# Kernel tuning notes

Measured on AMD Instinct MI355X. Metric: run time of the kernel, lower is better.

The kernel has to match this reference:

```python
import jax, jax.numpy as jnp
import numpy as np

N_NODES = 50000
N_EDGES = 800000
HIDDEN = 128
NUM_RBF = 32
N_GRAPHS = 500
VOCAB = 100


def setup_inputs() -> dict:
    key = jax.random.key(0)
    ks = jax.random.split(key, 16)
    x = jax.random.randint(ks[0], (N_NODES,), 0, VOCAB)
    edge_index = jax.random.randint(ks[1], (2, N_EDGES), 0, N_NODES)
    edge_attr = jax.random.normal(ks[2], (N_EDGES, NUM_RBF), dtype=jnp.float32)
    batch = jnp.sort(jax.random.randint(ks[3], (N_NODES,), 0, N_GRAPHS))
    zdim = 2 * HIDDEN + NUM_RBF
    s = 1.0 / np.sqrt(zdim)
    params = {"emb": jax.random.normal(ks[4], (VOCAB, HIDDEN), dtype=jnp.float32)}
    for l, k0 in zip((1, 2, 3), (5, 8, 11)):
        params[f"Wf{l}"] = jax.random.uniform(ks[k0], (zdim, HIDDEN), minval=-s, maxval=s, dtype=jnp.float32)
        params[f"bf{l}"] = jnp.zeros((HIDDEN,), dtype=jnp.float32)
        params[f"Ws{l}"] = jax.random.uniform(ks[k0 + 1], (zdim, HIDDEN), minval=-s, maxval=s, dtype=jnp.float32)
        params[f"bs{l}"] = jnp.zeros((HIDDEN,), dtype=jnp.float32)
    sl = 1.0 / np.sqrt(HIDDEN)
    params["Wlin"] = jax.random.uniform(ks[14], (HIDDEN, HIDDEN), minval=-sl, maxval=sl, dtype=jnp.float32)
    params["blin"] = jnp.zeros((HIDDEN,), dtype=jnp.float32)
    return {"x": x, "edge_index": edge_index, "edge_attr": edge_attr, "batch": batch, **params}


def _cgconv(h, src, dst, edge_attr, Wf, bf, Ws, bs):
    # z = [x_i || x_j || e_ij]; i = target (dst), j = source (src)
    z = jnp.concatenate([h[dst], h[src], edge_attr], axis=-1)  # [E, 2H+D]
    msg = jax.nn.sigmoid(z @ Wf + bf) * jax.nn.softplus(z @ Ws + bs)  # [E, H]
    agg = jax.ops.segment_sum(msg, dst, num_segments=N_NODES)
    return h + agg


def reference(x, edge_index, edge_attr, batch, emb,
              Wf1, bf1, Ws1, bs1, Wf2, bf2, Ws2, bs2, Wf3, bf3, Ws3, bs3,
              Wlin, blin):
    src, dst = edge_index[0], edge_index[1]
    h = emb[x]  # [N, H]
    h = jax.nn.relu(_cgconv(h, src, dst, edge_attr, Wf1, bf1, Ws1, bs1))
    h = jax.nn.relu(_cgconv(h, src, dst, edge_attr, Wf2, bf2, Ws2, bs2))
    h = jax.nn.relu(_cgconv(h, src, dst, edge_attr, Wf3, bf3, Ws3, bs3))
    sums = jax.ops.segment_sum(h, batch, num_segments=N_GRAPHS)  # [G, H]
    counts = jax.ops.segment_sum(jnp.ones((N_NODES,), h.dtype), batch, num_segments=N_GRAPHS)
    pooled = sums / jnp.maximum(counts, 1.0)[:, None]
    return pooled @ Wlin + blin
```

## Files before the change

### kernel.cpp

```cpp
#include <hip/hip_runtime.h>
#include <hip/hip_bf16.h>
#include <hip/hip_fp16.h>
#include <cstdint>
#include <cstddef>

#define NNODES 50000
#define NEDGES 800000
#define HID 128
#define NRBF 32
#define NGRAPH 500
#define NB_SCAN 196
#define EPB 64
#define NEBLK (NEDGES / EPB)
#define SROW 130

typedef __attribute__((ext_vector_type(8))) short short8;
typedef __attribute__((ext_vector_type(4))) float f32x4;

__device__ inline short f2bf(float x) {
  __hip_bfloat16 b = __float2bfloat16(x);
  return *reinterpret_cast<short*>(&b);
}

__device__ inline unsigned int pk_bf16(float a, float b) {
  unsigned int r;
  asm("v_cvt_pk_bf16_f32 %0, %1, %2" : "=v"(r) : "v"(a), "v"(b));
  return r;
}
__device__ inline unsigned int pk_f16(float a, float b) {
  unsigned int r;
  asm("v_cvt_pkrtz_f16_f32 %0, %1, %2" : "=v"(r) : "v"(a), "v"(b));
  return r;
}
__device__ inline unsigned int pk_add_f16(unsigned int a, unsigned int b) {
  unsigned int r;
  asm("v_pk_add_f16 %0, %1, %2" : "=v"(r) : "v"(a), "v"(b));
  return r;
}
__device__ inline float aexp2(float x) {
  float r;
  asm("v_exp_f32 %0, %1" : "=v"(r) : "v"(x));
  return r;
}
__device__ inline float alog2(float x) {
  float r;
  asm("v_log_f32 %0, %1" : "=v"(r) : "v"(x));
  return r;
}

#define SC_F (-1.4426950408889634f)
#define SC_S (1.4426950408889634f)

__global__ void prep_all(
    const float* __restrict__ Wf0, const float* __restrict__ Ws0,
    const float* __restrict__ bf0, const float* __restrict__ bs0,
    const float* __restrict__ Wf1, const float* __restrict__ Ws1,
    const float* __restrict__ bf1, const float* __restrict__ bs1,
    const float* __restrict__ Wf2, const float* __restrict__ Ws2,
    const float* __restrict__ bf2, const float* __restrict__ bs2,
    unsigned short* __restrict__ WtB3, unsigned short* __restrict__ WnB3,
    float* __restrict__ biasv3) {
  const int l = blockIdx.y;
  const float* Wf = (l == 0) ? Wf0 : ((l == 1) ? Wf1 : Wf2);
  const float* Ws = (l == 0) ? Ws0 : ((l == 1) ? Ws1 : Ws2);
  const float* bf = (l == 0) ? bf0 : ((l == 1) ? bf1 : bf2);
  const float* bs = (l == 0) ? bs0 : ((l == 1) ? bs1 : bs2);
  unsigned short* WtB = WtB3 + l * 8192;
  unsigned short* WnB = WnB3 + l * 65536;
  float* biasv = biasv3 + l * 256;

  int i0 = blockIdx.x * blockDim.x + threadIdx.x;
  if (i0 < 8192) {
    int i = i0;
    int j = i & 7, lane = (i >> 3) & 63, t = i >> 9;
    int q = lane >> 4, n = lane & 15;
    int k = q * 8 + j, c = (t & 7) * 16 + n;
    const float* W = (t < 8) ? Wf : Ws;
    const float sc = (t < 8) ? SC_F : SC_S;
    WtB[i] = (unsigned short)f2bf(W[(size_t)(256 + k) * HID + c] * sc);
  } else if (i0 < 8192 + 65536) {
    int i = i0 - 8192;
    int j = i & 7;
    int lane = (i >> 3) & 63;
    int tk = (i >> 9) & 3;
    int tc = i >> 11;
    int q = lane >> 4, n = lane & 15;
    int k = tk * 32 + q * 8 + j;
    float v;
    int which;
    if (tc < 16) {
      int g = tc >> 1;
      which = tc & 1;
      int c = g * 16 + n;
      const float* W = which ? Ws : Wf;
      v = W[(size_t)k * HID + c];
    } else {
      int g = (tc - 16) >> 1;
      which = (tc - 16) & 1;
      int c = g * 16 + n;
      const float* W = which ? Ws : Wf;
      v = W[(size_t)(128 + k) * HID + c];
    }
    WnB[i] = (unsigned short)f2bf(v * (which ? SC_S : SC_F));
    if (i < 256) {
      int c2 = i >> 1, w2 = i & 1;
      biasv[i] = w2 ? bs[c2] * SC_S : bf[c2] * SC_F;
    }
  }
}

__global__ void deg_hist(const int* __restrict__ dst, int* __restrict__ deg) {
  int e = blockIdx.x * blockDim.x + threadIdx.x;
  if (e < NEDGES) atomicAdd(&deg[dst[e]], 1);
}

__global__ __launch_bounds__(256) void scan_block(const int* __restrict__ deg, int* __restrict__ bsum) {
  __shared__ int s[256];
  int i = blockIdx.x * 256 + threadIdx.x;
  s[threadIdx.x] = (i < NNODES) ? deg[i] : 0;
  __syncthreads();
  for (int off = 128; off > 0; off >>= 1) {
    if (threadIdx.x < off) s[threadIdx.x] += s[threadIdx.x + off];
    __syncthreads();
  }
  if (threadIdx.x == 0) bsum[blockIdx.x] = s[0];
}

__global__ __launch_bounds__(256) void scan_top(const int* __restrict__ bsum,
                                                int* __restrict__ bpre) {
  __shared__ int s[256];
  int t = threadIdx.x;
  int v = (t < NB_SCAN) ? bsum[t] : 0;
  s[t] = v;
  __syncthreads();
  for (int off = 1; off < 256; off <<= 1) {
    int u = (t >= off) ? s[t - off] : 0;
    __syncthreads();
    s[t] += u;
    __syncthreads();
  }
  if (t < NB_SCAN) bpre[t] = s[t] - v;
}

__global__ __launch_bounds__(256) void scan_final(const int* __restrict__ deg,
                                                  const int* __restrict__ bpre,
                                                  int* __restrict__ cursor) {
  __shared__ int s[256];
  int i = blockIdx.x * 256 + threadIdx.x;
  int v = (i < NNODES) ? deg[i] : 0;
  s[threadIdx.x] = v;
  __syncthreads();
  for (int off = 1; off < 256; off <<= 1) {
    int t = (threadIdx.x >= off) ? s[threadIdx.x - off] : 0;
    __syncthreads();
    s[threadIdx.x] += t;
    __syncthreads();
  }
  if (i < NNODES) cursor[i] = bpre[blockIdx.x] + s[threadIdx.x] - v;
}

__global__ void scatter_edges_pack(const int* __restrict__ src, const int* __restrict__ dst,
                                   const float* __restrict__ eattr, int* __restrict__ cursor,
                                   int2* __restrict__ se2, unsigned short* __restrict__ eaB) {
  int e = blockIdx.x * blockDim.x + threadIdx.x;
  if (e >= NEDGES) return;
  int d = dst[e];
  int pos = atomicAdd(&cursor[d], 1);
  se2[pos] = make_int2(src[e], d);
  const float* ep = eattr + (size_t)e * NRBF;
  unsigned short* op = eaB + (size_t)pos * NRBF;
#pragma unroll
  for (int part = 0; part < 4; ++part) {
    const float4 v0 = *(const float4*)&ep[part * 8];
    const float4 v1 = *(const float4*)&ep[part * 8 + 4];
    uint4 o;
    o.x = pk_bf16(v0.x, v0.y);
    o.y = pk_bf16(v0.z, v0.w);
    o.z = pk_bf16(v1.x, v1.y);
    o.w = pk_bf16(v1.z, v1.w);
    *(uint4*)&op[part * 8] = o;
  }
}

__global__ __launch_bounds__(256) void node_mfma(
    const int* __restrict__ x, const float* __restrict__ emb,
    float* __restrict__ h, float* __restrict__ agg,
    const unsigned short* __restrict__ WnB, const float* __restrict__ biasv,
    unsigned int* __restrict__ Pdst, unsigned int* __restrict__ Psrc, int mode, int N) {
  const int tid = threadIdx.x;
  const int wv = tid >> 6;
  const int lane = tid & 63;
  const int q = lane >> 4;
  const int n = lane & 15;
  const int nb = blockIdx.x * 32 + (wv >> 1) * 16;
  const int srcwave = wv & 1;
  const int ctile0 = srcwave * 16;

  const bool valid = (nb + n) < N;
  int anode = nb + n;
  if (anode >= N) anode = N - 1;
  float* hp = h + (size_t)anode * HID;

  short8 a[4];
  if (mode == 0) {
    const float* ep = emb + (size_t)x[anode] * HID;
#pragma unroll
    for (int kt = 0; kt < 4; ++kt) {
      const float4 e0 = *(const float4*)&ep[kt * 32 + q * 8];
      const float4 e1 = *(const float4*)&ep[kt * 32 + q * 8 + 4];
      if (valid && !srcwave) {
        *(float4*)&hp[kt * 32 + q * 8] = e0;
        *(float4*)&hp[kt * 32 + q * 8 + 4] = e1;
      }
      union { short8 s8; unsigned int u32[4]; } au;
      au.u32[0] = pk_bf16(e0.x, e0.y);
      au.u32[1] = pk_bf16(e0.z, e0.w);
      au.u32[2] = pk_bf16(e1.x, e1.y);
      au.u32[3] = pk_bf16(e1.z, e1.w);
      a[kt] = au.s8;
    }
  } else {
    float* ap = agg + (size_t)anode * HID;
    float4 ev[8];
#pragma unroll
    for (int kt = 0; kt < 4; ++kt) {
      float4 e0 = *(const float4*)&hp[kt * 32 + q * 8];
      float4 e1 = *(const float4*)&hp[kt * 32 + q * 8 + 4];
      const float4 g0 = *(const float4*)&ap[kt * 32 + q * 8];
      const float4 g1 = *(const float4*)&ap[kt * 32 + q * 8 + 4];
      e0.x = fmaxf(e0.x + g0.x, 0.f); e0.y = fmaxf(e0.y + g0.y, 0.f);
      e0.z = fmaxf(e0.z + g0.z, 0.f); e0.w = fmaxf(e0.w + g0.w, 0.f);
      e1.x = fmaxf(e1.x + g1.x, 0.f); e1.y = fmaxf(e1.y + g1.y, 0.f);
      e1.z = fmaxf(e1.z + g1.z, 0.f); e1.w = fmaxf(e1.w + g1.w, 0.f);
      ev[2 * kt] = e0;
      ev[2 * kt + 1] = e1;
      union { short8 s8; unsigned int u32[4]; } au;
      au.u32[0] = pk_bf16(e0.x, e0.y);
      au.u32[1] = pk_bf16(e0.z, e0.w);
      au.u32[2] = pk_bf16(e1.x, e1.y);
      au.u32[3] = pk_bf16(e1.z, e1.w);
      a[kt] = au.s8;
    }
    __syncthreads();
    if (valid && !srcwave) {
      const float4 z4 = {0.f, 0.f, 0.f, 0.f};
#pragma unroll
      for (int kt = 0; kt < 4; ++kt) {
        *(float4*)&hp[kt * 32 + q * 8] = ev[2 * kt];
        *(float4*)&hp[kt * 32 + q * 8 + 4] = ev[2 * kt + 1];
        *(float4*)&ap[kt * 32 + q * 8] = z4;
        *(float4*)&ap[kt * 32 + q * 8 + 4] = z4;
      }
    }
  }

  const short8* WnB8 = (const short8*)WnB;
  f32x4 acc[16];
#pragma unroll
  for (int tc = 0; tc < 16; ++tc) acc[tc] = (f32x4){0.f, 0.f, 0.f, 0.f};

#pragma unroll
  for (int tc = 0; tc < 16; ++tc) {
#pragma unroll
    for (int kt = 0; kt < 4; ++kt) {
      short8 b = WnB8[((size_t)((ctile0 + tc) * 4 + kt)) * 64 + lane];
      acc[tc] = __builtin_amdgcn_mfma_f32_16x16x32_bf16(a[kt], b, acc[tc], 0, 0, 0);
    }
  }

  if (!srcwave) {
#pragma unroll
    for (int g2 = 0; g2 < 8; ++g2) {
      const int c = g2 * 16 + n;
      const float bvf = biasv[2 * c];
      const float bvs = biasv[2 * c + 1];
#pragma unroll
      for (int r = 0; r < 4; ++r) {
        int nd = nb + q * 4 + r;
        if (nd < N)
          Pdst[(size_t)nd * 128 + c] = pk_f16(acc[2 * g2][r] + bvf, acc[2 * g2 + 1][r] + bvs);
      }
    }
  } else {
#pragma unroll
    for (int g2 = 0; g2 < 8; ++g2) {
      const int c = g2 * 16 + n;
#pragma unroll
      for (int r = 0; r < 4; ++r) {
        int nd = nb + q * 4 + r;
        if (nd < N) Psrc[(size_t)nd * 128 + c] = pk_f16(acc[2 * g2][r], acc[2 * g2 + 1][r]);
      }
    }
  }
}

__global__ __launch_bounds__(256) void edge_mfma(
    const unsigned int* __restrict__ Pdst, const unsigned int* __restrict__ Psrc,
    const unsigned short* __restrict__ eaB, const unsigned short* __restrict__ WtB,
    const int2* __restrict__ se2, float* __restrict__ agg) {
  __shared__ unsigned int fsL[EPB * SROW];
  __shared__ int dstL[EPB];
  __shared__ int grpStart[EPB + 1];
  __shared__ int sndS;

  const int tid = threadIdx.x;
  const int base = blockIdx.x * EPB;
  const int lane = tid & 63;

  if (tid < EPB) {
    int2 sd = se2[base + tid];
    dstL[tid] = sd.y;
    int d = sd.y;
    int dprev = __shfl_up(d, 1);
    int flag = (tid == 0 || dprev != d) ? 1 : 0;
    unsigned long long mask = __ballot(flag);
    unsigned long long below = (lane == 63) ? ~0ull : ((1ull << (lane + 1)) - 1);
    int slot = __popcll(mask & below) - 1;
    if (flag) grpStart[slot] = tid;
    if (tid == 0) {
      int nd = __popcll(mask);
      sndS = nd;
      grpStart[nd] = EPB;
    }
  }

  const int wv = tid >> 6;
  const int q = lane >> 4;
  const int n = lane & 15;
  const int rowb = wv * 16 + q * 4;

  const short8 afrag = *(const short8*)&eaB[(size_t)(base + wv * 16 + n) * 32 + q * 8];

  const unsigned int* pp[4];
  const unsigned int* dp[4];
#pragma unroll
  for (int r = 0; r < 4; ++r) {
    const int2 sd = se2[base + rowb + r];
    pp[r] = Psrc + (size_t)sd.x * 128 + n;
    dp[r] = Pdst + (size_t)sd.y * 128 + n;
  }

  const short8* WtB8 = (const short8*)WtB;
  const f32x4 zero4 = {0.f, 0.f, 0.f, 0.f};
#pragma unroll
  for (int t = 0; t < 8; ++t) {
    unsigned int zpk[4];
#pragma unroll
    for (int r = 0; r < 4; ++r) zpk[r] = pk_add_f16(pp[r][t * 16], dp[r][t * 16]);
    short8 bfr = WtB8[t * 64 + lane];
    short8 bsr = WtB8[(8 + t) * 64 + lane];
    f32x4 cf = __builtin_amdgcn_mfma_f32_16x16x32_bf16(afrag, bfr, zero4, 0, 0, 0);
    f32x4 cs = __builtin_amdgcn_mfma_f32_16x16x32_bf16(afrag, bsr, zero4, 0, 0, 0);
#pragma unroll
    for (int r = 0; r < 4; ++r) {
      fsL[(rowb + r) * SROW + t * 16 + n] = pk_add_f16(pk_f16(cf[r], cs[r]), zpk[r]);
    }
  }
  __syncthreads();

  const int nd = sndS;
  for (int g = wv; g < nd; g += 4) {
    const int jb = grpStart[g];
    const int je = grpStart[g + 1];
    const int d = __builtin_amdgcn_readfirstlane(dstL[jb]);
    float acc0 = 0.f, acc1 = 0.f;

    uint2 pk_nx = *(const uint2*)&fsL[jb * SROW + 2 * lane];
    for (int j = jb; j < je; ++j) {
      const uint2 pk = pk_nx;
      int jn = (j + 1 < je) ? (j + 1) : j;
      pk_nx = *(const uint2*)&fsL[jn * SROW + 2 * lane];

      const float2 z0 = __half22float2(*reinterpret_cast<const __half2*>(&pk.x));
      const float2 z1 = __half22float2(*reinterpret_cast<const __half2*>(&pk.y));
      const float sig0 = __builtin_amdgcn_rcpf(1.f + aexp2(z0.x));
      const float sig1 = __builtin_amdgcn_rcpf(1.f + aexp2(z1.x));
      const float sp0 = fmaxf(z0.y, 0.f) + alog2(1.f + aexp2(fminf(z0.y, -z0.y)));
      const float sp1 = fmaxf(z1.y, 0.f) + alog2(1.f + aexp2(fminf(z1.y, -z1.y)));
      acc0 = fmaf(sig0, sp0, acc0);
      acc1 = fmaf(sig1, sp1, acc1);
    }
    acc0 *= 0.6931471805599453f;
    acc1 *= 0.6931471805599453f;
    float* ap = agg + (size_t)d * HID + 2 * lane;
    if (g == 0 || g == nd - 1) {
      atomicAdd(ap, acc0);
      atomicAdd(ap + 1, acc1);
    } else {
      *(float2*)ap = make_float2(acc0, acc1);
    }
  }
}

__global__ __launch_bounds__(256) void pool_kernel(
    const float* __restrict__ h, const float* __restrict__ agg,
    const int* __restrict__ batch, float* __restrict__ sums, float* __restrict__ counts) {
  __shared__ int gidL[64];
  __shared__ int grpS[65];
  __shared__ int sndP;

  const int tid = threadIdx.x;
  const int lane = tid & 63;
  const int wv = tid >> 6;
  const int nb = blockIdx.x * 64;
  int nvalid = NNODES - nb;
  if (nvalid > 64) nvalid = 64;

  if (tid < 64) {
    int node = nb + tid;
    int g = batch[node < NNODES ? node : NNODES - 1];
    gidL[tid] = g;
    int gprev = __shfl_up(g, 1);
    int flag = (tid < nvalid && (tid == 0 || gprev != g)) ? 1 : 0;
    unsigned long long mask = __ballot(flag);
    int slot = __popcll(mask & ((lane == 63) ? ~0ull : ((1ull << (lane + 1)) - 1))) - 1;
    if (flag) grpS[slot] = tid;
    if (tid == 0) {
      int nd = __popcll(mask);
      sndP = nd;
      grpS[nd] = nvalid;
    }
  }
  __syncthreads();

  const int nd = sndP;
  for (int g = wv; g < nd; g += 4) {
    const int jb = grpS[g];
    const int je = grpS[g + 1];
    const int gid = __builtin_amdgcn_readfirstlane(gidL[jb]);
    float a0 = 0.f, a1 = 0.f;
    for (int j = jb; j < je; ++j) {
      const float2 hv = *(const float2*)&h[(size_t)(nb + j) * HID + 2 * lane];
      const float2 av = *(const float2*)&agg[(size_t)(nb + j) * HID + 2 * lane];
      a0 += fmaxf(hv.x + av.x, 0.f);
      a1 += fmaxf(hv.y + av.y, 0.f);
    }
    float* sp = sums + (size_t)gid * HID + 2 * lane;
    const bool bnd = (g == 0 || g == nd - 1);
    if (bnd) {
      atomicAdd(sp, a0);
      atomicAdd(sp + 1, a1);
    } else {
      *(float2*)sp = make_float2(a0, a1);
    }
    if (lane == 0) {
      if (bnd) atomicAdd(&counts[gid], (float)(je - jb));
      else counts[gid] = (float)(je - jb);
    }
  }
}

__global__ __launch_bounds__(128) void final_kernel(
    const float* __restrict__ sums, const float* __restrict__ counts,
    const float* __restrict__ Wlin, const float* __restrict__ blin,
    float* __restrict__ out) {
  int g = blockIdx.x;
  int c = threadIdx.x;
  __shared__ float pool[HID];
  float cnt = counts[g];
  cnt = cnt > 1.f ? cnt : 1.f;
  pool[c] = sums[(size_t)g * HID + c] / cnt;
  __syncthreads();
  float acc = blin[c];
#pragma unroll 8
  for (int k = 0; k < HID; ++k) acc = fmaf(pool[k], Wlin[k * HID + c], acc);
  out[(size_t)g * HID + c] = acc;
}

extern "C" void kernel_launch(void* const* d_in, const int* in_sizes, int n_in,
                              void* d_out, int out_size, void* d_ws, size_t ws_size,
                              hipStream_t stream) {
  const int* x = (const int*)d_in[0];
  const int* eidx = (const int*)d_in[1];
  const float* eattr = (const float*)d_in[2];
  const int* batch = (const int*)d_in[3];
  const float* emb = (const float*)d_in[4];
  const float* Wf[3] = {(const float*)d_in[5], (const float*)d_in[9], (const float*)d_in[13]};
  const float* bf[3] = {(const float*)d_in[6], (const float*)d_in[10], (const float*)d_in[14]};
  const float* Ws[3] = {(const float*)d_in[7], (const float*)d_in[11], (const float*)d_in[15]};
  const float* bs[3] = {(const float*)d_in[8], (const float*)d_in[12], (const float*)d_in[16]};
  const float* Wlin = (const float*)d_in[17];
  const float* blin = (const float*)d_in[18];
  const int* srcp = eidx;
  const int* dstp = eidx + NEDGES;

  float* wsf = (float*)d_ws;
  float* h = wsf;
  float* PdstF = h + (size_t)NNODES * HID;
  float* agg = PdstF + (size_t)NNODES * 256;
  float* sums = agg + (size_t)NNODES * HID;
  float* counts = sums + (size_t)NGRAPH * HID;
  float* biasv3 = counts + NGRAPH;
  unsigned int* Psrc = (unsigned int*)(biasv3 + 768);
  unsigned short* WtB3 = (unsigned short*)(Psrc + (size_t)NNODES * 128);
  unsigned short* WnB3 = WtB3 + 3 * 8192;
  unsigned short* eaB = WnB3 + 3 * 65536;
  int2* se2 = (int2*)(eaB + (size_t)NEDGES * 32);
  int* deg = (int*)(se2 + NEDGES);
  int* cursor = deg + NNODES;
  int* bsum = cursor + NNODES;
  int* bpre = bsum + NB_SCAN;
  unsigned int* Pdst = (unsigned int*)PdstF;

  dim3 pgrid(288, 3);
  prep_all<<<pgrid, 256, 0, stream>>>(Wf[0], Ws[0], bf[0], bs[0],
                                      Wf[1], Ws[1], bf[1], bs[1],
                                      Wf[2], Ws[2], bf[2], bs[2],
                                      WtB3, WnB3, biasv3);

  hipMemsetAsync(deg, 0, NNODES * sizeof(int), stream);
  deg_hist<<<(NEDGES + 255) / 256, 256, 0, stream>>>(dstp, deg);
  scan_block<<<NB_SCAN, 256, 0, stream>>>(deg, bsum);
  scan_top<<<1, 256, 0, stream>>>(bsum, bpre);
  scan_final<<<NB_SCAN, 256, 0, stream>>>(deg, bpre, cursor);
  scatter_edges_pack<<<(NEDGES + 255) / 256, 256, 0, stream>>>(srcp, dstp, eattr, cursor,
                                                               se2, eaB);

  hipMemsetAsync(agg, 0, (size_t)NNODES * HID * sizeof(float), stream);

  const int nblk_node = (NNODES + 31) / 32;
  for (int l = 0; l < 3; ++l) {
    node_mfma<<<nblk_node, 256, 0, stream>>>(x, emb, h, agg, WnB3 + l * 65536,
                                             biasv3 + l * 256, Pdst, Psrc,
                                             l > 0 ? 1 : 0, NNODES);
    edge_mfma<<<NEBLK, 256, 0, stream>>>(Pdst, Psrc, eaB, WtB3 + l * 8192, se2, agg);
  }

  hipMemsetAsync(sums, 0, (size_t)(NGRAPH * HID + NGRAPH) * sizeof(float), stream);
  pool_kernel<<<(NNODES + 63) / 64, 256, 0, stream>>>(h, agg, batch, sums, counts);
  final_kernel<<<NGRAPH, 128, 0, stream>>>(sums, counts, Wlin, blin, (float*)d_out);
}
```

Measured before the change: 736.1 us.

## Permute node projection layout for vector stores and hoist dst projection per group

Node projection outputs are now stored in a permuted column layout so each lane writes two 16-byte vectors per node instead of scattered 4-byte stores. In the edge kernel, source projections are read as 16-byte vectors. The destination projection is no longer gathered per edge; it is loaded once per destination group and added during the reduction loop. This cuts per-edge gather traffic roughly in half, at the cost of an extra f16 add per element in the reduction loop and an index mapping that must stay consistent between the two kernels.

```diff
diff --git a/kernel.cpp b/kernel.cpp
--- a/kernel.cpp
+++ b/kernel.cpp
@@ -270,25 +270,31 @@
 
   if (!srcwave) {
 #pragma unroll
-    for (int g2 = 0; g2 < 8; ++g2) {
-      const int c = g2 * 16 + n;
-      const float bvf = biasv[2 * c];
-      const float bvs = biasv[2 * c + 1];
-#pragma unroll
-      for (int r = 0; r < 4; ++r) {
-        int nd = nb + q * 4 + r;
-        if (nd < N)
-          Pdst[(size_t)nd * 128 + c] = pk_f16(acc[2 * g2][r] + bvf, acc[2 * g2 + 1][r] + bvs);
+    for (int r = 0; r < 4; ++r) {
+      const int node = nb + q * 4 + r;
+      if (node < N) {
+        unsigned int o[8];
+#pragma unroll
+        for (int g2 = 0; g2 < 8; ++g2) {
+          const int c = g2 * 16 + n;
+          o[g2] = pk_f16(acc[2 * g2][r] + biasv[2 * c], acc[2 * g2 + 1][r] + biasv[2 * c + 1]);
+        }
+        *(uint4*)&Pdst[(size_t)node * 128 + n * 8] = make_uint4(o[0], o[1], o[2], o[3]);
+        *(uint4*)&Pdst[(size_t)node * 128 + n * 8 + 4] = make_uint4(o[4], o[5], o[6], o[7]);
       }
     }
   } else {
 #pragma unroll
-    for (int g2 = 0; g2 < 8; ++g2) {
-      const int c = g2 * 16 + n;
-#pragma unroll
-      for (int r = 0; r < 4; ++r) {
-        int nd = nb + q * 4 + r;
-        if (nd < N) Psrc[(size_t)nd * 128 + c] = pk_f16(acc[2 * g2][r], acc[2 * g2 + 1][r]);
+    for (int r = 0; r < 4; ++r) {
+      const int node = nb + q * 4 + r;
+      if (node < N) {
+        unsigned int o[8];
+#pragma unroll
+        for (int g2 = 0; g2 < 8; ++g2) {
+          o[g2] = pk_f16(acc[2 * g2][r], acc[2 * g2 + 1][r]);
+        }
+        *(uint4*)&Psrc[(size_t)node * 128 + n * 8] = make_uint4(o[0], o[1], o[2], o[3]);
+        *(uint4*)&Psrc[(size_t)node * 128 + n * 8 + 4] = make_uint4(o[4], o[5], o[6], o[7]);
       }
     }
   }
@@ -332,37 +338,44 @@
   const short8 afrag = *(const short8*)&eaB[(size_t)(base + wv * 16 + n) * 32 + q * 8];
 
   const unsigned int* pp[4];
-  const unsigned int* dp[4];
 #pragma unroll
   for (int r = 0; r < 4; ++r) {
-    const int2 sd = se2[base + rowb + r];
-    pp[r] = Psrc + (size_t)sd.x * 128 + n;
-    dp[r] = Pdst + (size_t)sd.y * 128 + n;
+    const int s = se2[base + rowb + r].x;
+    pp[r] = Psrc + (size_t)s * 128 + n * 8;
   }
 
   const short8* WtB8 = (const short8*)WtB;
   const f32x4 zero4 = {0.f, 0.f, 0.f, 0.f};
 #pragma unroll
-  for (int t = 0; t < 8; ++t) {
-    unsigned int zpk[4];
-#pragma unroll
-    for (int r = 0; r < 4; ++r) zpk[r] = pk_add_f16(pp[r][t * 16], dp[r][t * 16]);
-    short8 bfr = WtB8[t * 64 + lane];
-    short8 bsr = WtB8[(8 + t) * 64 + lane];
-    f32x4 cf = __builtin_amdgcn_mfma_f32_16x16x32_bf16(afrag, bfr, zero4, 0, 0, 0);
-    f32x4 cs = __builtin_amdgcn_mfma_f32_16x16x32_bf16(afrag, bsr, zero4, 0, 0, 0);
-#pragma unroll
-    for (int r = 0; r < 4; ++r) {
-      fsL[(rowb + r) * SROW + t * 16 + n] = pk_add_f16(pk_f16(cf[r], cs[r]), zpk[r]);
+  for (int half = 0; half < 2; ++half) {
+    uint4 ps4[4];
+#pragma unroll
+    for (int r = 0; r < 4; ++r) ps4[r] = *(const uint4*)&pp[r][half * 4];
+#pragma unroll
+    for (int tt = 0; tt < 4; ++tt) {
+      const int t = half * 4 + tt;
+      short8 bfr = WtB8[t * 64 + lane];
+      short8 bsr = WtB8[(8 + t) * 64 + lane];
+      f32x4 cf = __builtin_amdgcn_mfma_f32_16x16x32_bf16(afrag, bfr, zero4, 0, 0, 0);
+      f32x4 cs = __builtin_amdgcn_mfma_f32_16x16x32_bf16(afrag, bsr, zero4, 0, 0, 0);
+#pragma unroll
+      for (int r = 0; r < 4; ++r) {
+        const unsigned int psv = (tt == 0) ? ps4[r].x : (tt == 1) ? ps4[r].y
+                                : (tt == 2) ? ps4[r].z : ps4[r].w;
+        fsL[(rowb + r) * SROW + t * 16 + n] = pk_add_f16(pk_f16(cf[r], cs[r]), psv);
+      }
     }
   }
   __syncthreads();
 
   const int nd = sndS;
+  const int l7 = lane & 7, l3 = lane >> 3;
   for (int g = wv; g < nd; g += 4) {
     const int jb = grpStart[g];
     const int je = grpStart[g + 1];
     const int d = __builtin_amdgcn_readfirstlane(dstL[jb]);
+    const unsigned int pdx = Pdst[(size_t)d * 128 + 16 * l7 + l3];
+    const unsigned int pdy = Pdst[(size_t)d * 128 + 16 * l7 + 8 + l3];
     float acc0 = 0.f, acc1 = 0.f;
 
     uint2 pk_nx = *(const uint2*)&fsL[jb * SROW + 2 * lane];
@@ -371,8 +384,10 @@
       int jn = (j + 1 < je) ? (j + 1) : j;
       pk_nx = *(const uint2*)&fsL[jn * SROW + 2 * lane];
 
-      const float2 z0 = __half22float2(*reinterpret_cast<const __half2*>(&pk.x));
-      const float2 z1 = __half22float2(*reinterpret_cast<const __half2*>(&pk.y));
+      const unsigned int zx = pk_add_f16(pk.x, pdx);
+      const unsigned int zy = pk_add_f16(pk.y, pdy);
+      const float2 z0 = __half22float2(*reinterpret_cast<const __half2*>(&zx));
+      const float2 z1 = __half22float2(*reinterpret_cast<const __half2*>(&zy));
       const float sig0 = __builtin_amdgcn_rcpf(1.f + aexp2(z0.x));
       const float sig1 = __builtin_amdgcn_rcpf(1.f + aexp2(z1.x));
       const float sp0 = fmaxf(z0.y, 0.f) + alog2(1.f + aexp2(fminf(z0.y, -z0.y)));
```

Result: slower. 815.9 us (+10.8%).
